# Optimization experiments

Hardware: AMD Instinct MI355X
Metric: run time of the kernel (lower is better)

The kernel has to match this reference:

```python
import jax, jax.numpy as jnp
from jax import lax
import numpy as np
import math

jax.config.update('jax_enable_x64', True)

F32 = jnp.float32
F64 = jnp.float64
N_NODES = 100
K_NET = 7
EPS_SK = 0.1
GAMMA = 1.0
STOPERR = 1e-6
MAXIT = 50
RHO0 = 0.8
MASK_RATIO = 0.1
LEN_KEEP = int(N_NODES * (1.0 - MASK_RATIO))  # 90
NHEAD = 4
HDIM = N_NODES // NHEAD  # 25
TOTAL_EPOCH = 600

_SUBNET_MAP = {0: [1,2,3,4,5,6,7,8,9,51,52,53,54,55,56,57,58], 1: [10,11,12,13,14,15,59,60,61,62,63,64,65,66], 2: [16,17,18,19,20,21,22,23,67,68,69,70,71,72,73], 3: [24,25,26,27,28,29,30,74,75,76,77,78], 4: [31,32,33,79,80], 5: [34,35,36,37,81,82,83,84,85,86,87,88,89], 6: [38,39,40,41,42,43,44,45,46,47,48,49,50,90,91,92,93,94,95,96,97,98,99,100]}

def _subnet_mask():
    m = np.zeros((K_NET, N_NODES), dtype=np.float32)
    for k, idx in _SUBNET_MAP.items():
        m[k, np.array(idx) - 1] = 1.0
    return jnp.asarray(m)

SUBNET = _subnet_mask()  # [7,100] float
CLUSTER_PRIOR = jnp.asarray(np.array([17, 14, 15, 12, 5, 13, 24], np.float64)[:, None] / 100.0)  # [7,1] f64

def _sinusoid(n_pos, d):
    pos = np.arange(n_pos)[:, None].astype(np.float64)
    i = np.arange(d)[None, :]
    ang = pos / np.power(10000.0, 2 * (i // 2) / d)
    tab = np.zeros((n_pos, d))
    tab[:, 0::2] = np.sin(ang[:, 0::2])
    tab[:, 1::2] = np.cos(ang[:, 1::2])
    return jnp.asarray(tab[None], dtype=np.float32)

POS_EMBED = _sinusoid(N_NODES, N_NODES)  # [1,100,100]

def _ln(x, g, b, eps=1e-5):
    m = jnp.mean(x, -1, keepdims=True)
    v = jnp.mean((x - m) ** 2, -1, keepdims=True)
    return (x - m) / jnp.sqrt(v + eps) * g + b

def _layer(x, Wqkv, bqkv, Wo, bo, g1, bn1, W1, bf1, W2, bf2, g2, bn2):
    # torch TransformerEncoderLayer, post-LN, relu FFN, dropout ignored (eval)
    B, N, D = x.shape
    qkv = x @ Wqkv + bqkv                                  # [B,N,3D]
    q, k, v = jnp.split(qkv, 3, axis=-1)
    q = q.reshape(B, N, NHEAD, HDIM)
    k = k.reshape(B, N, NHEAD, HDIM)
    v = v.reshape(B, N, NHEAD, HDIM)
    s = jnp.einsum('bqhd,bkhd->bhqk', q, k) / math.sqrt(HDIM)
    a = jax.nn.softmax(s, axis=-1)
    o = jnp.einsum('bhqk,bkhd->bqhd', a, v).reshape(B, N, D)
    x = _ln(x + (o @ Wo + bo), g1, bn1)
    h = jax.nn.relu(x @ W1 + bf1) @ W2 + bf2
    return _ln(x + h, g2, bn2)

def _blocks(x, ps):
    for l in range(2):  # depth=2 (fixed, structural)
        x = _layer(x, *(p[l] for p in ps))
    return x

def _normalize(x):
    return x / jnp.maximum(jnp.linalg.norm(x, axis=-1, keepdims=True), 1e-12)

def _sinkhorn_batch(cost, rho):
    # Sequential over batch with b carried across samples (self.b persistence in torch)
    costd = cost.astype(F64)
    n = N_NODES
    Pa = jnp.full((n, 1), 1.0 / n, dtype=F64)
    Pb = jnp.concatenate([rho * CLUSTER_PRIOR, jnp.array([[1.0 - rho]], F64)], axis=0)  # [8,1]
    fi = GAMMA / (GAMMA + EPS_SK)
    def step(b0, Pm):
        P = -jax.nn.log_softmax(Pm, axis=1)                # [100,7]
        ex = jnp.concatenate([P, jnp.zeros((n, 1), F64)], axis=1)  # [100,8]
        Q = jnp.exp(-ex / EPS_SK)
        def cond(st):
            return (st[2] > STOPERR) & (st[3] < MAXIT)
        def body(st):
            _, b, _, it = st
            a = Pa / (Q @ b)
            b2 = Pb / (Q.T @ a)
            b2 = b2.at[:-1].set(b2[:-1] ** fi)             # semi_use
            return (a, b2, jnp.linalg.norm(b2 - b), it + 1)
        a, b, _, _ = lax.while_loop(cond, body, (jnp.zeros((n, 1), F64), b0, jnp.asarray(1.0, F64), 0))
        plan = n * a * Q * b.T
        return b, plan[:, :-1].astype(F32)
    b_init = jnp.full((K_NET + 1, 1), 1.0 / (K_NET + 1), dtype=F64)
    _, Qs = lax.scan(step, b_init, costd)
    return Qs  # [B,100,7] f32

def _forward(imgs, Wqkv, bqkv, Wo, bo, ln1_g, ln1_b, W1, b1, W2, b2, ln2_g, ln2_b, mask_token, pW1, pb1, pW2, pb2, rand_K, epoch):
    sg = lax.stop_gradient
    imgs = imgs.astype(F32)
    B = imgs.shape[0]
    ps = (Wqkv, bqkv, Wo, bo, ln1_g, ln1_b, W1, b1, W2, b2, ln2_g, ln2_b)
    rho = RHO0 + (1.0 - RHO0) * math.exp(-5.0 * (1.0 - epoch / TOTAL_EPOCH) ** 2)
    # ---- cost from EMA features (entirely no-grad in torch) ----
    feat = _blocks(sg(imgs), tuple(sg(p) for p in ps))     # [B,100,100]
    denom = SUBNET.sum(-1, keepdims=True) + 1e-6           # [7,1]
    subnet_feat = jnp.einsum('kn,bnd->bkd', SUBNET, feat) / denom
    cost = jnp.einsum('bnd,bkd->bnk', _normalize(feat), _normalize(subnet_feat))  # [B,100,7]
    # ---- P2OT assignment (Sinkhorn fixed point per sample) ----
    Q = _sinkhorn_batch(cost, rho)                         # [B,100,7]
    quality = Q.sum(-1)                                    # [B,100]
    thr = jnp.quantile(quality, 1.0 - rho, axis=1, keepdims=True)
    low = quality < thr
    noise = jnp.where(low, jnp.zeros((), F32), jnp.einsum('bnk,bk->bn', Q, sg(rand_K)))
    ids_shuffle = jnp.argsort(noise, axis=1)               # stable ascending
    ids_keep = ids_shuffle[:, :LEN_KEEP]
    ids_restore = jnp.argsort(ids_shuffle, axis=1)
    mask = jnp.ones((B, N_NODES), F32).at[jnp.arange(B)[:, None], ids_keep].set(0.0)
    x_masked = jnp.take_along_axis(sg(imgs), ids_keep[:, :, None], axis=1)  # detached gather (no_grad)
    # ---- encoder + prediction head ----
    n_mask = N_NODES + 1 - LEN_KEEP                        # 11, as in torch (last token unused)
    mask_tokens = jnp.broadcast_to(mask_token.astype(F32), (B, n_mask, N_NODES))
    x_ = jnp.concatenate([x_masked, mask_tokens], axis=1)  # [B,101,100]
    idx = jnp.broadcast_to(ids_restore[:, :, None], (B, N_NODES, N_NODES))
    x = jnp.take_along_axis(x_, idx, axis=1)
    x = x + POS_EMBED
    x = _blocks(x, ps)
    pred = jax.nn.leaky_relu(x @ pW1 + pb1, 0.01) @ pW2 + pb2
    mse = jnp.mean((pred - imgs) ** 2, axis=-1)            # [B,100]
    return jnp.sum(mse * mask) / jnp.sum(mask)

def setup_inputs() -> dict:
    key = jax.random.key(0)
    ks = jax.random.split(key, 12)
    B, D, FF, PH = 256, 100, 2048, 1024
    s = 0.05
    return {
        'imgs': jax.random.normal(ks[0], (B, D, D), F32),
        'Wqkv': jax.random.normal(ks[1], (2, D, 3 * D), F32) * s,
        'bqkv': jnp.zeros((2, 3 * D), F32),
        'Wo': jax.random.normal(ks[2], (2, D, D), F32) * s,
        'bo': jnp.zeros((2, D), F32),
        'ln1_g': jnp.ones((2, D), F32),
        'ln1_b': jnp.zeros((2, D), F32),
        'W1': jax.random.normal(ks[3], (2, D, FF), F32) * s,
        'b1': jnp.zeros((2, FF), F32),
        'W2': jax.random.normal(ks[4], (2, FF, D), F32) * s,
        'b2': jnp.zeros((2, D), F32),
        'ln2_g': jnp.ones((2, D), F32),
        'ln2_b': jnp.zeros((2, D), F32),
        'mask_token': jax.random.normal(ks[5], (1, 1, D), F32) * 0.14,
        'pW1': jax.random.normal(ks[6], (D, PH), F32) * s,
        'pb1': jnp.zeros((PH,), F32),
        'pW2': jax.random.normal(ks[7], (PH, D), F32) * s,
        'pb2': jnp.zeros((D,), F32),
        'rand_K': jax.random.uniform(ks[8], (B, K_NET), F32),
        'epoch': 100,
    }

def reference(imgs, Wqkv, bqkv, Wo, bo, ln1_g, ln1_b, W1, b1, W2, b2, ln2_g, ln2_b, mask_token, pW1, pb1, pW2, pb2, rand_K, epoch):
    return _forward(imgs, Wqkv, bqkv, Wo, bo, ln1_g, ln1_b, W1, b1, W2, b2, ln2_g, ln2_b, mask_token, pW1, pb1, pW2, pb2, rand_K, epoch)
```

## Files before the change

kernel.cpp:

```cpp
#include <hip/hip_runtime.h>
#include <cmath>
#include <cfloat>

#define B_   256
#define N_   100
#define D_   100
#define BN_  25600

typedef _Float16 f16;
typedef _Float16 f16x8 __attribute__((ext_vector_type(8)));
typedef float    f32x4 __attribute__((ext_vector_type(4)));

__device__ const int d_node2k[100] = {
 0,0,0,0,0,0,0,0,0,
 1,1,1,1,1,1,
 2,2,2,2,2,2,2,2,
 3,3,3,3,3,3,3,
 4,4,4,
 5,5,5,5,
 6,6,6,6,6,6,6,6,6,6,6,6,6,
 0,0,0,0,0,0,0,0,
 1,1,1,1,1,1,1,1,
 2,2,2,2,2,2,2,
 3,3,3,3,3,
 4,4,
 5,5,5,5,5,5,5,5,5,
 6,6,6,6,6,6,6,6,6,6,6};

__device__ __forceinline__ double get_rho(int epoch){
    double t = 1.0 - (double)epoch / 600.0;
    return 0.8 + (1.0 - 0.8) * exp(-5.0 * t * t);
}

__global__ void k_pos_embed(float* pose){
    int idx = blockIdx.x * blockDim.x + threadIdx.x;
    if (idx >= N_ * D_) return;
    int n = idx / D_;
    int i = idx - n * D_;
    double expo = (double)(2 * (i / 2)) / (double)D_;
    double ang  = (double)n / pow(10000.0, expo);
    pose[idx] = (float)((i & 1) ? cos(ang) : sin(ang));
}

__global__ __launch_bounds__(256) void k_prep_a(const float* __restrict__ W,
        const float* __restrict__ bias, f16* __restrict__ WT, int N, int NP){
    int idx = blockIdx.x * 256 + threadIdx.x;
    if (idx >= NP * 128) return;
    int n = idx >> 7, k = idx & 127;
    float v = 0.f;
    if (n < N){
        if (k < 100) v = W[(size_t)k * N + n];
        else if (k == 100) v = bias[n];
    }
    WT[idx] = (f16)v;
}

__global__ __launch_bounds__(256) void k_prep_b(const float* __restrict__ W,
        f16* __restrict__ WT, int F, int lg2F){
    int idx = blockIdx.x * 256 + threadIdx.x;
    if (idx >= 112 * F) return;
    int f = idx & (F - 1);
    int d = idx >> lg2F;
    WT[(size_t)d * F + f] = (d < 100) ? (f16)W[(size_t)f * 100 + d] : (f16)0.f;
}

template<int RT, bool F16OUT>
__global__ __launch_bounds__(128, 2) void k_gemm16(
        const float* __restrict__ x, const f16* __restrict__ WT,
        float* __restrict__ outf, f16* __restrict__ outh, int N){
    __shared__ f16 wls[4 * 112 * 32];
    int tid = threadIdx.x;
    int wv = tid >> 6, lane = tid & 63;
    int l15 = lane & 15, lg = lane >> 4;
    int row0 = blockIdx.x * (RT * 32) + wv * (RT * 16);
    int c0 = blockIdx.y * 112;

    for (int c = tid; c < 1792; c += 128){
        int n = c >> 4, k8 = c & 15;
        uint4 v = *(const uint4*)(WT + (size_t)(c0 + n) * 128 + k8 * 8);
        *(uint4*)((char*)wls + (k8 >> 2) * 7168 + n * 64 + (((k8 & 3) * 16) ^ ((n & 3) << 4))) = v;
    }

    f16x8 xf[RT][4];
    #pragma unroll
    for (int rt = 0; rt < RT; ++rt){
        const float* xr = x + (size_t)(row0 + rt * 16 + l15) * 100;
        #pragma unroll
        for (int ks = 0; ks < 3; ++ks){
            int k0 = ks * 32 + lg * 8;
            float4 a = *(const float4*)(xr + k0);
            float4 b = *(const float4*)(xr + k0 + 4);
            f16 t[8] = {(f16)a.x,(f16)a.y,(f16)a.z,(f16)a.w,(f16)b.x,(f16)b.y,(f16)b.z,(f16)b.w};
            xf[rt][ks] = *(const f16x8*)t;
        }
        if (lg == 0){
            float4 a = *(const float4*)(xr + 96);
            f16 t[8] = {(f16)a.x,(f16)a.y,(f16)a.z,(f16)a.w,(f16)1.f,(f16)0.f,(f16)0.f,(f16)0.f};
            xf[rt][3] = *(const f16x8*)t;
        } else {
            f16 t[8] = {(f16)0.f,(f16)0.f,(f16)0.f,(f16)0.f,(f16)0.f,(f16)0.f,(f16)0.f,(f16)0.f};
            xf[rt][3] = *(const f16x8*)t;
        }
    }
    __syncthreads();

    f32x4 acc[RT][7];
    #pragma unroll
    for (int rt = 0; rt < RT; ++rt)
        #pragma unroll
        for (int ct = 0; ct < 7; ++ct) acc[rt][ct] = (f32x4)0.f;

    #pragma unroll
    for (int ks = 0; ks < 4; ++ks){
        #pragma unroll
        for (int ct = 0; ct < 7; ++ct){
            int n = ct * 16 + l15;
            f16x8 a = *(const f16x8*)((char*)wls + ks * 7168 + n * 64 + ((lg * 16) ^ ((n & 3) << 4)));
            #pragma unroll
            for (int rt = 0; rt < RT; ++rt)
                acc[rt][ct] = __builtin_amdgcn_mfma_f32_16x16x32_f16(a, xf[rt][ks], acc[rt][ct], 0, 0, 0);
        }
    }

    #pragma unroll
    for (int rt = 0; rt < RT; ++rt){
        int r = row0 + rt * 16 + l15;
        #pragma unroll
        for (int ct = 0; ct < 7; ++ct){
            int col = c0 + ct * 16 + lg * 4;
            if (col + 4 <= N){
                if (F16OUT){
                    f16 t[4] = {(f16)acc[rt][ct][0], (f16)acc[rt][ct][1],
                                (f16)acc[rt][ct][2], (f16)acc[rt][ct][3]};
                    *(uint2*)(outh + (size_t)r * N + col) = *(const uint2*)t;
                } else {
                    *(f32x4*)(outf + (size_t)r * N + col) = acc[rt][ct];
                }
            }
        }
    }
}

template<int ACT>
__global__ __launch_bounds__(128, 2) void k_ffn2(
        const float* __restrict__ x, const f16* __restrict__ WaT,
        const f16* __restrict__ WbT, float* __restrict__ Pbase, int F){
    __shared__ f16 waTs[4 * 32 * 32];
    __shared__ f16 wbTs[112 * 32];
    __shared__ f16 hs[2 * 64 * 32];
    int tid = threadIdx.x;
    int wv = tid >> 6, lane = tid & 63;
    int l15 = lane & 15, lg = lane >> 4;
    int row0 = blockIdx.x * 128 + wv * 64;
    int fh = blockIdx.y;
    int Fh = F >> 1;
    float* P = Pbase + (size_t)fh * 2560000;

    f16x8 xf[4][4];
    #pragma unroll
    for (int rt = 0; rt < 4; ++rt){
        const float* xr = x + (size_t)(row0 + rt * 16 + l15) * 100;
        #pragma unroll
        for (int ks = 0; ks < 3; ++ks){
            int k0 = ks * 32 + lg * 8;
            float4 a = *(const float4*)(xr + k0);
            float4 b = *(const float4*)(xr + k0 + 4);
            f16 t[8] = {(f16)a.x,(f16)a.y,(f16)a.z,(f16)a.w,(f16)b.x,(f16)b.y,(f16)b.z,(f16)b.w};
            xf[rt][ks] = *(const f16x8*)t;
        }
        if (lg == 0){
            float4 a = *(const float4*)(xr + 96);
            f16 t[8] = {(f16)a.x,(f16)a.y,(f16)a.z,(f16)a.w,(f16)1.f,(f16)0.f,(f16)0.f,(f16)0.f};
            xf[rt][3] = *(const f16x8*)t;
        } else {
            f16 t[8] = {(f16)0.f,(f16)0.f,(f16)0.f,(f16)0.f,(f16)0.f,(f16)0.f,(f16)0.f,(f16)0.f};
            xf[rt][3] = *(const f16x8*)t;
        }
    }

    f32x4 acc[4][7];
    #pragma unroll
    for (int rt = 0; rt < 4; ++rt)
        #pragma unroll
        for (int ct = 0; ct < 7; ++ct) acc[rt][ct] = (f32x4)0.f;

    int nch = Fh >> 5;
    for (int ch = 0; ch < nch; ++ch){
        int f0 = fh * Fh + ch * 32;
        __syncthreads();
        for (int c = tid; c < 512; c += 128){
            int f = c >> 4, k8 = c & 15;
            uint4 v = *(const uint4*)(WaT + (size_t)(f0 + f) * 128 + k8 * 8);
            *(uint4*)((char*)waTs + (k8 >> 2) * 2048 + f * 64 + (((k8 & 3) * 16) ^ ((f & 3) << 4))) = v;
        }
        for (int c = tid; c < 448; c += 128){
            int d = c >> 2, s = c & 3;
            uint4 v = *(const uint4*)(WbT + (size_t)d * F + f0 + s * 8);
            *(uint4*)((char*)wbTs + d * 64 + ((s * 16) ^ ((d & 3) << 4))) = v;
        }
        __syncthreads();

        #pragma unroll
        for (int ctp = 0; ctp < 2; ++ctp){
            f32x4 h[4];
            #pragma unroll
            for (int rt = 0; rt < 4; ++rt) h[rt] = (f32x4)0.f;
            #pragma unroll
            for (int ks = 0; ks < 4; ++ks){
                int fl = ctp * 16 + l15;
                f16x8 a = *(const f16x8*)((char*)waTs + ks * 2048 + fl * 64 + ((lg * 16) ^ ((fl & 3) << 4)));
                #pragma unroll
                for (int rt = 0; rt < 4; ++rt)
                    h[rt] = __builtin_amdgcn_mfma_f32_16x16x32_f16(a, xf[rt][ks], h[rt], 0, 0, 0);
            }
            #pragma unroll
            for (int rt = 0; rt < 4; ++rt){
                f16 t[4];
                #pragma unroll
                for (int reg = 0; reg < 4; ++reg){
                    float v = h[rt][reg];
                    v = (v > 0.f) ? v : (ACT ? 0.01f * v : 0.f);
                    t[reg] = (f16)v;
                }
                int xr = rt * 16 + l15;
                *(uint2*)((char*)hs + wv * 4096 + xr * 64 + ((ctp * 32 + lg * 8) ^ ((xr & 3) << 4))) = *(const uint2*)t;
            }
        }
        f16x8 bf[4];
        #pragma unroll
        for (int rt = 0; rt < 4; ++rt){
            int xr = rt * 16 + l15;
            bf[rt] = *(const f16x8*)((char*)hs + wv * 4096 + xr * 64 + ((lg * 16) ^ ((xr & 3) << 4)));
        }
        #pragma unroll
        for (int ct = 0; ct < 7; ++ct){
            int d = ct * 16 + l15;
            f16x8 a2 = *(const f16x8*)((char*)wbTs + d * 64 + ((lg * 16) ^ ((d & 3) << 4)));
            #pragma unroll
            for (int rt = 0; rt < 4; ++rt)
                acc[rt][ct] = __builtin_amdgcn_mfma_f32_16x16x32_f16(a2, bf[rt], acc[rt][ct], 0, 0, 0);
        }
    }

    #pragma unroll
    for (int rt = 0; rt < 4; ++rt){
        int r = row0 + rt * 16 + l15;
        #pragma unroll
        for (int ct = 0; ct < 7; ++ct){
            int col = ct * 16 + lg * 4;
            if (col < 100)
                *(f32x4*)(P + (size_t)r * 100 + col) = acc[rt][ct];
        }
    }
}

__global__ __launch_bounds__(128) void k_attn(const f16* __restrict__ qkv,
                                              float* __restrict__ o){
    int b = blockIdx.x >> 2;
    int h = blockIdx.x & 3;
    __shared__ float ks[100][26];
    __shared__ float vs[100][26];
    for (int i = threadIdx.x; i < 2500; i += 128){
        int n = i / 25, d = i - n * 25;
        const f16* base = qkv + (size_t)(b * 100 + n) * 300 + h * 25 + d;
        ks[n][d] = (float)base[100];
        vs[n][d] = (float)base[200];
    }
    __syncthreads();
    int n = threadIdx.x;
    if (n < 100){
        float q[25];
        const f16* qb = qkv + (size_t)(b * 100 + n) * 300 + h * 25;
        #pragma unroll
        for (int d = 0; d < 25; ++d) q[d] = (float)qb[d];
        float m = -FLT_MAX, l = 0.f, acc[25];
        #pragma unroll
        for (int d = 0; d < 25; ++d) acc[d] = 0.f;
        for (int c = 0; c < 100; ++c){
            float s = 0.f;
            #pragma unroll
            for (int d = 0; d < 25; ++d) s += q[d] * ks[c][d];
            s *= 0.2f;
            if (s <= m){
                float p = expf(s - m);
                l += p;
                #pragma unroll
                for (int d = 0; d < 25; ++d) acc[d] += p * vs[c][d];
            } else {
                float sc = expf(m - s);
                l = l * sc + 1.f;
                #pragma unroll
                for (int d = 0; d < 25; ++d) acc[d] = acc[d] * sc + vs[c][d];
                m = s;
            }
        }
        float inv = 1.f / l;
        float* ob = o + (size_t)(b * 100 + n) * 100 + h * 25;
        #pragma unroll
        for (int d = 0; d < 25; ++d) ob[d] = acc[d] * inv;
    }
}

__global__ __launch_bounds__(256) void k_add_ln(
        const float* __restrict__ xa, const float* __restrict__ xb,
        const float* __restrict__ xc, const float* __restrict__ bias,
        const float* __restrict__ g, const float* __restrict__ bt,
        float* __restrict__ out){
    int row  = blockIdx.x * 4 + (threadIdx.x >> 6);
    int lane = threadIdx.x & 63;
    const float* pa = xa + (size_t)row * 100;
    const float* pb = xb + (size_t)row * 100;
    int e1 = lane + 64;
    float v0 = pa[lane] + pb[lane];
    float v1 = (e1 < 100) ? (pa[e1] + pb[e1]) : 0.f;
    if (xc){
        const float* pc = xc + (size_t)row * 100;
        v0 += pc[lane];
        if (e1 < 100) v1 += pc[e1];
    }
    if (bias){
        v0 += bias[lane];
        if (e1 < 100) v1 += bias[e1];
    }
    float s = v0 + v1;
    #pragma unroll
    for (int m = 32; m >= 1; m >>= 1) s += __shfl_xor(s, m, 64);
    float mean = s / 100.f;
    float d0 = v0 - mean;
    float d1 = (e1 < 100) ? (v1 - mean) : 0.f;
    float s2 = d0 * d0 + d1 * d1;
    #pragma unroll
    for (int m = 32; m >= 1; m >>= 1) s2 += __shfl_xor(s2, m, 64);
    float rstd = 1.f / sqrtf(s2 / 100.f + 1e-5f);
    float* po = out + (size_t)row * 100;
    po[lane] = d0 * rstd * g[lane] + bt[lane];
    if (e1 < 100) po[e1] = d1 * rstd * g[e1] + bt[e1];
}

__global__ __launch_bounds__(256) void k_subnet_cost(const float* __restrict__ feat,
                                                     float* __restrict__ cost){
    int b = blockIdx.x;
    __shared__ float fs[100][101];
    __shared__ float sf[7][101];
    __shared__ float nf[100];
    __shared__ float ns[7];
    int tid = threadIdx.x;
    for (int idx = tid; idx < 10000; idx += 256){
        int n = idx / 100, d = idx - n * 100;
        fs[n][d] = feat[(size_t)(b * 100 + n) * 100 + d];
    }
    __syncthreads();
    const float cnt[7] = {17.f, 14.f, 15.f, 12.f, 5.f, 13.f, 24.f};
    for (int idx = tid; idx < 700; idx += 256){
        int k = idx / 100, d = idx - k * 100;
        float s = 0.f;
        for (int n = 0; n < 100; ++n) if (d_node2k[n] == k) s += fs[n][d];
        sf[k][d] = s / (cnt[k] + 1e-6f);
    }
    __syncthreads();
    if (tid < 100){
        float s = 0.f;
        for (int d = 0; d < 100; ++d) s += fs[tid][d] * fs[tid][d];
        float nv = sqrtf(s);
        nf[tid] = nv > 1e-12f ? nv : 1e-12f;
    }
    if (tid >= 128 && tid < 135){
        int k = tid - 128;
        float s = 0.f;
        for (int d = 0; d < 100; ++d) s += sf[k][d] * sf[k][d];
        float nv = sqrtf(s);
        ns[k] = nv > 1e-12f ? nv : 1e-12f;
    }
    __syncthreads();
    for (int idx = tid; idx < 700; idx += 256){
        int n = idx / 7, k = idx - n * 7;
        float s = 0.f;
        for (int d = 0; d < 100; ++d) s += fs[n][d] * sf[k][d];
        cost[(size_t)b * 700 + n * 7 + k] = s / (nf[n] * ns[k]);
    }
}

__global__ __launch_bounds__(128) void k_sinkhorn(const float* __restrict__ cost,
        float* __restrict__ qplan, float* __restrict__ qual,
        const int* __restrict__ ep){
    int b   = blockIdx.x;
    int tid = threadIdx.x;
    __shared__ double Qm[100][8];
    __shared__ double av[100];
    __shared__ double bv[8];
    __shared__ double b2v[8];
    __shared__ int s_stop;
    double rho = get_rho(ep[0]);
    const double prior[7] = {17.0/100.0, 14.0/100.0, 15.0/100.0, 12.0/100.0,
                             5.0/100.0, 13.0/100.0, 24.0/100.0};
    if (tid < 100){
        double c[7]; double mx = -1e300;
        for (int k = 0; k < 7; ++k){
            c[k] = (double)cost[(size_t)b * 700 + tid * 7 + k];
            if (c[k] > mx) mx = c[k];
        }
        double se = 0.0;
        for (int k = 0; k < 7; ++k) se += exp(c[k] - mx);
        double lse = mx + log(se);
        for (int k = 0; k < 7; ++k) Qm[tid][k] = exp(-((lse - c[k]) / 0.1));
        Qm[tid][7] = 1.0;
    }
    if (tid < 8) bv[tid] = 1.0 / 8.0;
    if (tid == 0) s_stop = 0;
    __syncthreads();
    const double fi = 1.0 / 1.1;
    int j = tid >> 4, l16 = tid & 15;
    double Pbj = (j < 7) ? rho * prior[j] : (1.0 - rho);
    for (int it = 0; it < 50; ++it){
        if (tid < 100){
            double s = 0.0;
            #pragma unroll
            for (int k = 0; k < 8; ++k) s += Qm[tid][k] * bv[k];
            av[tid] = 0.01 / s;
        }
        __syncthreads();
        double p = 0.0;
        for (int n = l16; n < 100; n += 16) p += Qm[n][j] * av[n];
        p += __shfl_xor(p, 8, 16);
        p += __shfl_xor(p, 4, 16);
        p += __shfl_xor(p, 2, 16);
        p += __shfl_xor(p, 1, 16);
        if (l16 == 0){
            double nb = Pbj / p;
            if (j < 7) nb = pow(nb, fi);
            b2v[j] = nb;
        }
        __syncthreads();
        if (tid == 0){
            double e2 = 0.0;
            #pragma unroll
            for (int k = 0; k < 8; ++k){
                double d = b2v[k] - bv[k];
                e2 += d * d;
                bv[k] = b2v[k];
            }
            s_stop = (e2 <= 1e-12) ? 1 : 0;
        }
        __syncthreads();
        if (s_stop) break;
    }
    if (tid < 100){
        float q = 0.f;
        for (int k = 0; k < 7; ++k){
            double pl = 100.0 * av[tid] * Qm[tid][k] * bv[k];
            float pf = (float)pl;
            qplan[(size_t)b * 700 + tid * 7 + k] = pf;
            q += pf;
        }
        qual[(size_t)b * 100 + tid] = q;
    }
}

__global__ __launch_bounds__(128) void k_select(const float* __restrict__ qual,
        const float* __restrict__ qplan, const float* __restrict__ randK,
        const int* __restrict__ ep, float* __restrict__ maskb){
    int b   = blockIdx.x;
    int tid = threadIdx.x;
    __shared__ float qs[100];
    __shared__ float sorted_s[100];
    __shared__ float noise_s[100];
    __shared__ float thr_f;
    if (tid < 100) qs[tid] = qual[(size_t)b * 100 + tid];
    __syncthreads();
    if (tid < 100){
        float q = qs[tid];
        int cl = 0, ce = 0;
        for (int m = 0; m < 100; ++m){ cl += (qs[m] < q); ce += (qs[m] == q); }
        for (int r2 = cl; r2 < cl + ce; ++r2) sorted_s[r2] = q;
    }
    __syncthreads();
    if (tid == 0){
        double rho = get_rho(ep[0]);
        double pos = (1.0 - rho) * 99.0;
        int lo = (int)floor(pos);
        if (lo > 98) lo = 98; if (lo < 0) lo = 0;
        double fr = pos - (double)lo;
        double thr = (double)sorted_s[lo] + ((double)sorted_s[lo + 1] - (double)sorted_s[lo]) * fr;
        thr_f = (float)thr;
    }
    __syncthreads();
    if (tid < 100){
        float nz = 0.f;
        if (!(qs[tid] < thr_f)){
            for (int k = 0; k < 7; ++k)
                nz += qplan[(size_t)b * 700 + tid * 7 + k] * randK[b * 7 + k];
        }
        noise_s[tid] = nz;
    }
    __syncthreads();
    if (tid < 100){
        float nz = noise_s[tid];
        int rk = 0;
        for (int m = 0; m < 100; ++m){
            rk += (noise_s[m] < nz);
            rk += ((noise_s[m] == nz) && (m < tid));
        }
        maskb[(size_t)b * 100 + tid] = (rk >= 90) ? 1.f : 0.f;
    }
}

__global__ void k_build_x(const float* __restrict__ imgs, const float* __restrict__ mtok,
        const float* __restrict__ maskb, const float* __restrict__ pose,
        float* __restrict__ x){
    int idx = blockIdx.x * 256 + threadIdx.x;
    if (idx >= B_ * N_ * D_) return;
    int d  = idx % 100;
    int bn = idx / 100;
    int n  = bn % 100;
    float v = (maskb[bn] == 0.f) ? imgs[idx] : mtok[d];
    x[idx] = v + pose[n * 100 + d];
}

__global__ __launch_bounds__(256) void k_loss(const float* __restrict__ p1,
        const float* __restrict__ p2, const float* __restrict__ pb2,
        const float* __restrict__ imgs, const float* __restrict__ maskb,
        double* __restrict__ partial){
    int wv   = threadIdx.x >> 6;
    int row  = blockIdx.x * 4 + wv;
    int lane = threadIdx.x & 63;
    const float* pp = p1 + (size_t)row * 100;
    const float* pq = p2 + (size_t)row * 100;
    const float* pi = imgs + (size_t)row * 100;
    float d0 = pp[lane] + pq[lane] + pb2[lane] - pi[lane];
    float s = d0 * d0;
    int e1 = lane + 64;
    if (e1 < 100){
        float d1 = pp[e1] + pq[e1] + pb2[e1] - pi[e1];
        s += d1 * d1;
    }
    #pragma unroll
    for (int m = 32; m >= 1; m >>= 1) s += __shfl_xor(s, m, 64);
    __shared__ float ls[4], lc[4];
    if (lane == 0){
        float mk = maskb[row];
        ls[wv] = (s / 100.f) * mk;
        lc[wv] = mk;
    }
    __syncthreads();
    if (threadIdx.x == 0){
        partial[2 * blockIdx.x]     = (double)(ls[0] + ls[1] + ls[2] + ls[3]);
        partial[2 * blockIdx.x + 1] = (double)(lc[0] + lc[1] + lc[2] + lc[3]);
    }
}

__global__ __launch_bounds__(256) void k_final(const double* __restrict__ partial,
                                               float* __restrict__ out){
    int tid = threadIdx.x;
    double s = 0.0, c = 0.0;
    for (int i = tid; i < 6400; i += 256){
        s += partial[2 * i];
        c += partial[2 * i + 1];
    }
    #pragma unroll
    for (int m = 32; m >= 1; m >>= 1){
        s += __shfl_xor(s, m, 64);
        c += __shfl_xor(c, m, 64);
    }
    __shared__ double ss[4], cs[4];
    if ((tid & 63) == 0){ ss[tid >> 6] = s; cs[tid >> 6] = c; }
    __syncthreads();
    if (tid == 0){
        double S = ss[0] + ss[1] + ss[2] + ss[3];
        double C = cs[0] + cs[1] + cs[2] + cs[3];
        out[0] = (float)(S / C);
    }
}

extern "C" void kernel_launch(void* const* d_in, const int* in_sizes, int n_in,
                              void* d_out, int out_size, void* d_ws, size_t ws_size,
                              hipStream_t stream){
    const float* imgs = (const float*)d_in[0];
    const float* Wqkv = (const float*)d_in[1];
    const float* bqkv = (const float*)d_in[2];
    const float* Wo   = (const float*)d_in[3];
    const float* bo   = (const float*)d_in[4];
    const float* ln1g = (const float*)d_in[5];
    const float* ln1b = (const float*)d_in[6];
    const float* W1   = (const float*)d_in[7];
    const float* b1   = (const float*)d_in[8];
    const float* W2   = (const float*)d_in[9];
    const float* b2   = (const float*)d_in[10];
    const float* ln2g = (const float*)d_in[11];
    const float* ln2b = (const float*)d_in[12];
    const float* mtok = (const float*)d_in[13];
    const float* pW1  = (const float*)d_in[14];
    const float* pb1  = (const float*)d_in[15];
    const float* pW2  = (const float*)d_in[16];
    const float* pb2  = (const float*)d_in[17];
    const float* rndK = (const float*)d_in[18];
    const int*   epoch = (const int*)d_in[19];

    float* ws   = (float*)d_ws;
    float* Xb   = ws;
    float* P1   = Xb + 2560000;
    float* P2   = P1 + 2560000;
    f16*   QKVh = (f16*)(P2 + 2560000);
    float* COSTb  = P2 + 2560000;
    float* QPLANb = COSTb + 179200;
    float* QUALb  = QPLANb + 179200;
    float* WARENA = P2 + 2560000 + 3840000;
    f16* wh = (f16*)WARENA;
    f16* WqkvT0 = wh;               wh += 43008;
    f16* WqkvT1 = wh;               wh += 43008;
    f16* WoT0   = wh;               wh += 14336;
    f16* WoT1   = wh;               wh += 14336;
    f16* W1T0   = wh;               wh += 262144;
    f16* W1T1   = wh;               wh += 262144;
    f16* W2T0   = wh;               wh += 229376;
    f16* W2T1   = wh;               wh += 229376;
    f16* PW1T   = wh;               wh += 131072;
    f16* PW2T   = wh;               wh += 114688;
    float* tail = WARENA + 671744;
    float* MASKb = tail;            tail += 25600;
    float* POSEb = tail;            tail += 10000;
    double* LOSSP = (double*)tail;

    k_prep_a<<<168,  256, 0, stream>>>(Wqkv,          bqkv,       WqkvT0, 300, 336);
    k_prep_a<<<168,  256, 0, stream>>>(Wqkv + 30000,  bqkv + 300, WqkvT1, 300, 336);
    k_prep_a<<<56,   256, 0, stream>>>(Wo,            bo,         WoT0,   100, 112);
    k_prep_a<<<56,   256, 0, stream>>>(Wo + 10000,    bo + 100,   WoT1,   100, 112);
    k_prep_a<<<1024, 256, 0, stream>>>(W1,            b1,         W1T0,  2048, 2048);
    k_prep_a<<<1024, 256, 0, stream>>>(W1 + 204800,   b1 + 2048,  W1T1,  2048, 2048);
    k_prep_b<<<896,  256, 0, stream>>>(W2,          W2T0, 2048, 11);
    k_prep_b<<<896,  256, 0, stream>>>(W2 + 204800, W2T1, 2048, 11);
    k_prep_a<<<512,  256, 0, stream>>>(pW1, pb1, PW1T, 1024, 1024);
    k_prep_b<<<448,  256, 0, stream>>>(pW2, PW2T, 1024, 10);
    k_pos_embed<<<79, 128, 0, stream>>>(POSEb);

    auto layer = [&](const float* xi, float* xo, int l){
        k_gemm16<4, true><<<dim3(200, 3), 128, 0, stream>>>(
            xi, l ? WqkvT1 : WqkvT0, nullptr, QKVh, 300);
        k_attn<<<1024, 128, 0, stream>>>(QKVh, P1);
        k_gemm16<2, false><<<dim3(400, 1), 128, 0, stream>>>(
            P1, l ? WoT1 : WoT0, P2, nullptr, 100);
        k_add_ln<<<6400, 256, 0, stream>>>(xi, P2, nullptr, nullptr,
            ln1g + l * 100, ln1b + l * 100, xo);
        k_ffn2<0><<<dim3(200, 2), 128, 0, stream>>>(
            xo, l ? W1T1 : W1T0, l ? W2T1 : W2T0, P1, 2048);
        k_add_ln<<<6400, 256, 0, stream>>>(xo, P1, P2, b2 + l * 100,
            ln2g + l * 100, ln2b + l * 100, xo);
    };

    layer(imgs, Xb, 0);
    layer(Xb, Xb, 1);

    k_subnet_cost<<<256, 256, 0, stream>>>(Xb, COSTb);
    k_sinkhorn<<<256, 128, 0, stream>>>(COSTb, QPLANb, QUALb, epoch);
    k_select<<<256, 128, 0, stream>>>(QUALb, QPLANb, rndK, epoch, MASKb);

    k_build_x<<<10000, 256, 0, stream>>>(imgs, mtok, MASKb, POSEb, Xb);

    layer(Xb, Xb, 0);
    layer(Xb, Xb, 1);

    k_ffn2<1><<<dim3(200, 2), 128, 0, stream>>>(Xb, PW1T, PW2T, P1, 1024);

    k_loss<<<6400, 256, 0, stream>>>(P1, P2, pb2, imgs, MASKb, LOSSP);
    k_final<<<1, 256, 0, stream>>>(LOSSP, (float*)d_out);
}
```

Before: 1.109 ms.

## Split FFN hidden dimension four ways with 64-wide chunks and row-major swizzled LDS

The fused FFN kernel now splits the hidden dimension across four grid slices instead of two and processes 64-wide hidden chunks per iteration. Its four partial outputs are summed in the add+LayerNorm and loss kernels, which now read P1..P4. Weight tiles in LDS move to a row-major layout with an 8-way XOR swizzle. The QKV GEMM uses smaller row tiles with twice as many blocks, and the occupancy hints on launch bounds are dropped. The aim is more parallelism and fewer barriers per hidden unit, at the cost of extra partial-sum memory traffic and more shared memory per block.

```diff
diff --git a/kernel.cpp b/kernel.cpp
--- a/kernel.cpp
+++ b/kernel.cpp
@@ -65,10 +65,10 @@
 }
 
 template<int RT, bool F16OUT>
-__global__ __launch_bounds__(128, 2) void k_gemm16(
+__global__ __launch_bounds__(128) void k_gemm16(
         const float* __restrict__ x, const f16* __restrict__ WT,
         float* __restrict__ outf, f16* __restrict__ outh, int N){
-    __shared__ f16 wls[4 * 112 * 32];
+    __shared__ f16 wls[112 * 128];
     int tid = threadIdx.x;
     int wv = tid >> 6, lane = tid & 63;
     int l15 = lane & 15, lg = lane >> 4;
@@ -76,9 +76,9 @@
     int c0 = blockIdx.y * 112;
 
     for (int c = tid; c < 1792; c += 128){
-        int n = c >> 4, k8 = c & 15;
-        uint4 v = *(const uint4*)(WT + (size_t)(c0 + n) * 128 + k8 * 8);
-        *(uint4*)((char*)wls + (k8 >> 2) * 7168 + n * 64 + (((k8 & 3) * 16) ^ ((n & 3) << 4))) = v;
+        int n = c >> 4, slot = c & 15;
+        uint4 v = *(const uint4*)(WT + (size_t)(c0 + n) * 128 + slot * 8);
+        *(uint4*)((char*)wls + n * 256 + ((slot * 16) ^ ((n & 7) << 4))) = v;
     }
 
     f16x8 xf[RT][4];
@@ -115,7 +115,7 @@
         #pragma unroll
         for (int ct = 0; ct < 7; ++ct){
             int n = ct * 16 + l15;
-            f16x8 a = *(const f16x8*)((char*)wls + ks * 7168 + n * 64 + ((lg * 16) ^ ((n & 3) << 4)));
+            f16x8 a = *(const f16x8*)((char*)wls + n * 256 + ((ks * 64 + lg * 16) ^ ((n & 7) << 4)));
             #pragma unroll
             for (int rt = 0; rt < RT; ++rt)
                 acc[rt][ct] = __builtin_amdgcn_mfma_f32_16x16x32_f16(a, xf[rt][ks], acc[rt][ct], 0, 0, 0);
@@ -142,19 +142,18 @@
 }
 
 template<int ACT>
-__global__ __launch_bounds__(128, 2) void k_ffn2(
+__global__ __launch_bounds__(128) void k_ffn2(
         const float* __restrict__ x, const f16* __restrict__ WaT,
         const f16* __restrict__ WbT, float* __restrict__ Pbase, int F){
-    __shared__ f16 waTs[4 * 32 * 32];
-    __shared__ f16 wbTs[112 * 32];
-    __shared__ f16 hs[2 * 64 * 32];
+    __shared__ f16 waTs[64 * 128];
+    __shared__ f16 wbTs[112 * 64];
+    __shared__ f16 hs[2 * 64 * 64];
     int tid = threadIdx.x;
     int wv = tid >> 6, lane = tid & 63;
     int l15 = lane & 15, lg = lane >> 4;
     int row0 = blockIdx.x * 128 + wv * 64;
-    int fh = blockIdx.y;
-    int Fh = F >> 1;
-    float* P = Pbase + (size_t)fh * 2560000;
+    int Fq = F >> 2;
+    float* P = Pbase + (size_t)blockIdx.y * 2560000;
 
     f16x8 xf[4][4];
     #pragma unroll
@@ -184,31 +183,31 @@
         #pragma unroll
         for (int ct = 0; ct < 7; ++ct) acc[rt][ct] = (f32x4)0.f;
 
-    int nch = Fh >> 5;
+    int nch = Fq >> 6;
     for (int ch = 0; ch < nch; ++ch){
-        int f0 = fh * Fh + ch * 32;
+        int f0 = blockIdx.y * Fq + ch * 64;
         __syncthreads();
-        for (int c = tid; c < 512; c += 128){
-            int f = c >> 4, k8 = c & 15;
-            uint4 v = *(const uint4*)(WaT + (size_t)(f0 + f) * 128 + k8 * 8);
-            *(uint4*)((char*)waTs + (k8 >> 2) * 2048 + f * 64 + (((k8 & 3) * 16) ^ ((f & 3) << 4))) = v;
-        }
-        for (int c = tid; c < 448; c += 128){
-            int d = c >> 2, s = c & 3;
+        for (int c = tid; c < 1024; c += 128){
+            int f = c >> 4, slot = c & 15;
+            uint4 v = *(const uint4*)(WaT + (size_t)(f0 + f) * 128 + slot * 8);
+            *(uint4*)((char*)waTs + f * 256 + ((slot * 16) ^ ((f & 7) << 4))) = v;
+        }
+        for (int c = tid; c < 896; c += 128){
+            int d = c >> 3, s = c & 7;
             uint4 v = *(const uint4*)(WbT + (size_t)d * F + f0 + s * 8);
-            *(uint4*)((char*)wbTs + d * 64 + ((s * 16) ^ ((d & 3) << 4))) = v;
+            *(uint4*)((char*)wbTs + d * 128 + ((s * 16) ^ ((d & 7) << 4))) = v;
         }
         __syncthreads();
 
         #pragma unroll
-        for (int ctp = 0; ctp < 2; ++ctp){
+        for (int ctp = 0; ctp < 4; ++ctp){
             f32x4 h[4];
             #pragma unroll
             for (int rt = 0; rt < 4; ++rt) h[rt] = (f32x4)0.f;
             #pragma unroll
             for (int ks = 0; ks < 4; ++ks){
                 int fl = ctp * 16 + l15;
-                f16x8 a = *(const f16x8*)((char*)waTs + ks * 2048 + fl * 64 + ((lg * 16) ^ ((fl & 3) << 4)));
+                f16x8 a = *(const f16x8*)((char*)waTs + fl * 256 + ((ks * 64 + lg * 16) ^ ((fl & 7) << 4)));
                 #pragma unroll
                 for (int rt = 0; rt < 4; ++rt)
                     h[rt] = __builtin_amdgcn_mfma_f32_16x16x32_f16(a, xf[rt][ks], h[rt], 0, 0, 0);
@@ -223,22 +222,25 @@
                     t[reg] = (f16)v;
                 }
                 int xr = rt * 16 + l15;
-                *(uint2*)((char*)hs + wv * 4096 + xr * 64 + ((ctp * 32 + lg * 8) ^ ((xr & 3) << 4))) = *(const uint2*)t;
+                *(uint2*)((char*)hs + wv * 8192 + xr * 128 + ((ctp * 32 + lg * 8) ^ ((xr & 7) << 4))) = *(const uint2*)t;
             }
         }
-        f16x8 bf[4];
-        #pragma unroll
-        for (int rt = 0; rt < 4; ++rt){
-            int xr = rt * 16 + l15;
-            bf[rt] = *(const f16x8*)((char*)hs + wv * 4096 + xr * 64 + ((lg * 16) ^ ((xr & 3) << 4)));
-        }
-        #pragma unroll
-        for (int ct = 0; ct < 7; ++ct){
-            int d = ct * 16 + l15;
-            f16x8 a2 = *(const f16x8*)((char*)wbTs + d * 64 + ((lg * 16) ^ ((d & 3) << 4)));
-            #pragma unroll
-            for (int rt = 0; rt < 4; ++rt)
-                acc[rt][ct] = __builtin_amdgcn_mfma_f32_16x16x32_f16(a2, bf[rt], acc[rt][ct], 0, 0, 0);
+        #pragma unroll
+        for (int ks2 = 0; ks2 < 2; ++ks2){
+            f16x8 bf[4];
+            #pragma unroll
+            for (int rt = 0; rt < 4; ++rt){
+                int xr = rt * 16 + l15;
+                bf[rt] = *(const f16x8*)((char*)hs + wv * 8192 + xr * 128 + ((ks2 * 64 + lg * 16) ^ ((xr & 7) << 4)));
+            }
+            #pragma unroll
+            for (int ct = 0; ct < 7; ++ct){
+                int d = ct * 16 + l15;
+                f16x8 a2 = *(const f16x8*)((char*)wbTs + d * 128 + ((ks2 * 64 + lg * 16) ^ ((d & 7) << 4)));
+                #pragma unroll
+                for (int rt = 0; rt < 4; ++rt)
+                    acc[rt][ct] = __builtin_amdgcn_mfma_f32_16x16x32_f16(a2, bf[rt], acc[rt][ct], 0, 0, 0);
+            }
         }
     }
 
@@ -302,39 +304,39 @@
 }
 
 __global__ __launch_bounds__(256) void k_add_ln(
-        const float* __restrict__ xa, const float* __restrict__ xb,
-        const float* __restrict__ xc, const float* __restrict__ bias,
+        const float* __restrict__ xa, const float* __restrict__ p1,
+        const float* __restrict__ p2, const float* __restrict__ p3,
+        const float* __restrict__ p4, const float* __restrict__ bias,
         const float* __restrict__ g, const float* __restrict__ bt,
         float* __restrict__ out){
     int row  = blockIdx.x * 4 + (threadIdx.x >> 6);
     int lane = threadIdx.x & 63;
-    const float* pa = xa + (size_t)row * 100;
-    const float* pb = xb + (size_t)row * 100;
+    size_t off = (size_t)row * 100;
     int e1 = lane + 64;
-    float v0 = pa[lane] + pb[lane];
-    float v1 = (e1 < 100) ? (pa[e1] + pb[e1]) : 0.f;
-    if (xc){
-        const float* pc = xc + (size_t)row * 100;
-        v0 += pc[lane];
-        if (e1 < 100) v1 += pc[e1];
+    bool has1 = e1 < 100;
+    float v0 = xa[off + lane] + p1[off + lane];
+    float v1 = has1 ? (xa[off + e1] + p1[off + e1]) : 0.f;
+    if (p2){
+        v0 += p2[off + lane] + p3[off + lane] + p4[off + lane];
+        if (has1) v1 += p2[off + e1] + p3[off + e1] + p4[off + e1];
     }
     if (bias){
         v0 += bias[lane];
-        if (e1 < 100) v1 += bias[e1];
+        if (has1) v1 += bias[e1];
     }
     float s = v0 + v1;
     #pragma unroll
     for (int m = 32; m >= 1; m >>= 1) s += __shfl_xor(s, m, 64);
     float mean = s / 100.f;
     float d0 = v0 - mean;
-    float d1 = (e1 < 100) ? (v1 - mean) : 0.f;
+    float d1 = has1 ? (v1 - mean) : 0.f;
     float s2 = d0 * d0 + d1 * d1;
     #pragma unroll
     for (int m = 32; m >= 1; m >>= 1) s2 += __shfl_xor(s2, m, 64);
     float rstd = 1.f / sqrtf(s2 / 100.f + 1e-5f);
-    float* po = out + (size_t)row * 100;
+    float* po = out + off;
     po[lane] = d0 * rstd * g[lane] + bt[lane];
-    if (e1 < 100) po[e1] = d1 * rstd * g[e1] + bt[e1];
+    if (has1) po[e1] = d1 * rstd * g[e1] + bt[e1];
 }
 
 __global__ __launch_bounds__(256) void k_subnet_cost(const float* __restrict__ feat,
@@ -517,20 +519,19 @@
 }
 
 __global__ __launch_bounds__(256) void k_loss(const float* __restrict__ p1,
-        const float* __restrict__ p2, const float* __restrict__ pb2,
+        const float* __restrict__ p2, const float* __restrict__ p3,
+        const float* __restrict__ p4, const float* __restrict__ pb2,
         const float* __restrict__ imgs, const float* __restrict__ maskb,
         double* __restrict__ partial){
     int wv   = threadIdx.x >> 6;
     int row  = blockIdx.x * 4 + wv;
     int lane = threadIdx.x & 63;
-    const float* pp = p1 + (size_t)row * 100;
-    const float* pq = p2 + (size_t)row * 100;
-    const float* pi = imgs + (size_t)row * 100;
-    float d0 = pp[lane] + pq[lane] + pb2[lane] - pi[lane];
+    size_t off = (size_t)row * 100;
+    float d0 = p1[off+lane] + p2[off+lane] + p3[off+lane] + p4[off+lane] + pb2[lane] - imgs[off+lane];
     float s = d0 * d0;
     int e1 = lane + 64;
     if (e1 < 100){
-        float d1 = pp[e1] + pq[e1] + pb2[e1] - pi[e1];
+        float d1 = p1[off+e1] + p2[off+e1] + p3[off+e1] + p4[off+e1] + pb2[e1] - imgs[off+e1];
         s += d1 * d1;
     }
     #pragma unroll
@@ -599,11 +600,13 @@
     float* Xb   = ws;
     float* P1   = Xb + 2560000;
     float* P2   = P1 + 2560000;
-    f16*   QKVh = (f16*)(P2 + 2560000);
-    float* COSTb  = P2 + 2560000;
+    float* P3   = P2 + 2560000;
+    float* P4   = P3 + 2560000;
+    f16*   QKVh = (f16*)P3;
+    float* COSTb  = P4 + 2560000;
     float* QPLANb = COSTb + 179200;
     float* QUALb  = QPLANb + 179200;
-    float* WARENA = P2 + 2560000 + 3840000;
+    float* WARENA = QUALb + 25600;
     f16* wh = (f16*)WARENA;
     f16* WqkvT0 = wh;               wh += 43008;
     f16* WqkvT1 = wh;               wh += 43008;
@@ -633,16 +636,16 @@
     k_pos_embed<<<79, 128, 0, stream>>>(POSEb);
 
     auto layer = [&](const float* xi, float* xo, int l){
-        k_gemm16<4, true><<<dim3(200, 3), 128, 0, stream>>>(
+        k_gemm16<2, true><<<dim3(400, 3), 128, 0, stream>>>(
             xi, l ? WqkvT1 : WqkvT0, nullptr, QKVh, 300);
         k_attn<<<1024, 128, 0, stream>>>(QKVh, P1);
         k_gemm16<2, false><<<dim3(400, 1), 128, 0, stream>>>(
             P1, l ? WoT1 : WoT0, P2, nullptr, 100);
-        k_add_ln<<<6400, 256, 0, stream>>>(xi, P2, nullptr, nullptr,
-            ln1g + l * 100, ln1b + l * 100, xo);
-        k_ffn2<0><<<dim3(200, 2), 128, 0, stream>>>(
+        k_add_ln<<<6400, 256, 0, stream>>>(xi, P2, nullptr, nullptr, nullptr,
+            nullptr, ln1g + l * 100, ln1b + l * 100, xo);
+        k_ffn2<0><<<dim3(200, 4), 128, 0, stream>>>(
             xo, l ? W1T1 : W1T0, l ? W2T1 : W2T0, P1, 2048);
-        k_add_ln<<<6400, 256, 0, stream>>>(xo, P1, P2, b2 + l * 100,
+        k_add_ln<<<6400, 256, 0, stream>>>(xo, P1, P2, P3, P4, b2 + l * 100,
             ln2g + l * 100, ln2b + l * 100, xo);
     };
 
@@ -658,8 +661,8 @@
     layer(Xb, Xb, 0);
     layer(Xb, Xb, 1);
 
-    k_ffn2<1><<<dim3(200, 2), 128, 0, stream>>>(Xb, PW1T, PW2T, P1, 1024);
-
-    k_loss<<<6400, 256, 0, stream>>>(P1, P2, pb2, imgs, MASKb, LOSSP);
+    k_ffn2<1><<<dim3(200, 4), 128, 0, stream>>>(Xb, PW1T, PW2T, P1, 1024);
+
+    k_loss<<<6400, 256, 0, stream>>>(P1, P2, P3, P4, pb2, imgs, MASKb, LOSSP);
     k_final<<<1, 256, 0, stream>>>(LOSSP, (float*)d_out);
 }
```

Measured after the change: 1.182 ms. +6.6%, slower.
